# Kernel optimization log

Hardware: AMD Instinct MI355X
Metric: run time of the kernel (lower is better)

Reference implementation:

```python
import jax, jax.numpy as jnp
import numpy as np

N, E, CIN, COUT, KS, DIM = 10000, 160000, 64, 128, 5, 3
EPS = 1e-5


def spline_conv(x, src, dst, pseudo, W, Wr, bias, K):
    """SplineConv (degree=1, open spline, aggr='mean', root_weight, bias).
    x: [N, Cin]; pseudo: [E, DIM] in [0,1]; W: [K**DIM, Cin, Cout].
    For each edge, the degree-1 open B-spline basis has 2**DIM nonzero
    kernel entries. We scatter basis-weighted source features into a
    [N, K**DIM, Cin] accumulator, then contract with W in one GEMM.
    """
    n, cin = x.shape
    ktot = K ** DIM
    v = pseudo * (K - 1)                      # [E, DIM]
    bot = jnp.floor(v)
    frac = v - bot                            # fractional position in cell
    boti = bot.astype(jnp.int32)
    x_src = x[src]                            # gather [E, Cin]
    acc = jnp.zeros((n * ktot, cin), x.dtype)
    for combo in range(2 ** DIM):             # 8 fixed spline corners
        bits = [(combo >> d) & 1 for d in range(DIM)]
        w = jnp.ones((pseudo.shape[0],), x.dtype)
        idx = jnp.zeros((pseudo.shape[0],), jnp.int32)
        for d in range(DIM):
            w = w * (frac[:, d] if bits[d] else 1.0 - frac[:, d])
            idx = idx * K + jnp.clip(boti[:, d] + bits[d], 0, K - 1)
        acc = acc.at[dst * ktot + idx].add(w[:, None] * x_src)
    msg = jnp.einsum('nki,kio->no', acc.reshape(n, ktot, cin), W)
    deg = jnp.zeros((n,), x.dtype).at[dst].add(1.0)  # mean aggregation
    return msg / jnp.maximum(deg, 1.0)[:, None] + x @ Wr + bias


def batch_norm(x, g, b):
    # BatchNorm1d, training-mode batch statistics over the node dim
    mu = x.mean(0)
    var = x.var(0)
    return (x - mu) * jax.lax.rsqrt(var + EPS) * g + b


def setup_inputs() -> dict:
    key = jax.random.key(0)
    ks = jax.random.split(key, 16)
    ktot = KS ** DIM
    s1 = 1.0 / np.sqrt(CIN)
    s2 = 1.0 / np.sqrt(COUT)
    return {
        'x': jax.random.normal(ks[0], (N, CIN), jnp.float32),
        'edge_index': jax.random.randint(ks[1], (2, E), 0, N, jnp.int32),
        'edge_attr': jax.random.uniform(ks[2], (E, DIM), jnp.float32),
        'W1': jax.random.normal(ks[3], (ktot, CIN, COUT), jnp.float32) * s1,
        'Wr1': jax.random.normal(ks[4], (CIN, COUT), jnp.float32) * s1,
        'b1': jnp.zeros((COUT,), jnp.float32),
        'g1': jnp.ones((COUT,), jnp.float32),
        'be1': jnp.zeros((COUT,), jnp.float32),
        'W2': jax.random.normal(ks[5], (ktot, COUT, COUT), jnp.float32) * s2,
        'Wr2': jax.random.normal(ks[6], (COUT, COUT), jnp.float32) * s2,
        'b2': jnp.zeros((COUT,), jnp.float32),
        'g2': jnp.ones((COUT,), jnp.float32),
        'be2': jnp.zeros((COUT,), jnp.float32),
        'Wsc': jax.random.normal(ks[7], (1, CIN, COUT), jnp.float32) * s1,
        'Wrsc': jax.random.normal(ks[8], (CIN, COUT), jnp.float32) * s1,
        'bsc': jnp.zeros((COUT,), jnp.float32),
        'gsc': jnp.ones((COUT,), jnp.float32),
        'besc': jnp.zeros((COUT,), jnp.float32),
    }


def reference(x, edge_index, edge_attr, W1, Wr1, b1, g1, be1,
              W2, Wr2, b2, g2, be2, Wsc, Wrsc, bsc, gsc, besc):
    src, dst = edge_index[0], edge_index[1]
    # left branch: conv1 -> bn1 -> elu -> conv2 -> bn2
    h = spline_conv(x, src, dst, edge_attr, W1, Wr1, b1, KS)
    h = jax.nn.elu(batch_norm(h, g1, be1))
    h = batch_norm(spline_conv(h, src, dst, edge_attr, W2, Wr2, b2, KS), g2, be2)
    # shortcut: kernel_size=1 SplineConv -> bn
    s = batch_norm(spline_conv(x, src, dst, edge_attr, Wsc, Wrsc, bsc, 1), gsc, besc)
    return jax.nn.elu(h + s)
```

## Files before the change

kernel.cpp:

```cpp
#include <hip/hip_runtime.h>

#define N_NODES 10000
#define N_EDGES 160000
#define CIN 64
#define COUT 128
#define KTOT 125
#define NBINS (N_NODES * KTOT)
#define NPAIRS (N_EDGES * 8)
#define EPS 1e-5f
#define SPL 18
#define CH 3520
#define NSCB 40

#define CDIV(a,b) (((a)+(b)-1)/(b))

typedef __attribute__((ext_vector_type(8))) short short8;
typedef __attribute__((ext_vector_type(4))) float floatx4;

static __device__ __forceinline__ unsigned short f2b(float f) {
  union { float f; unsigned u; } v; v.f = f;
  unsigned r = v.u + 0x7FFFu + ((v.u >> 16) & 1u);
  return (unsigned short)(r >> 16);
}
static __device__ __forceinline__ float b2f(unsigned short u) {
  union { unsigned u; float f; } v; v.u = ((unsigned)u) << 16;
  return v.f;
}

typedef __attribute__((address_space(1))) const unsigned int guint;
typedef __attribute__((address_space(3))) unsigned int luint;
static __device__ __forceinline__ void ld_g2l16(const void* g, void* l) {
  __builtin_amdgcn_global_load_lds((guint*)g, (luint*)l, 16, 0, 0);
}

__global__ void ecount(const int* __restrict__ dst, int* __restrict__ ecnt, int E) {
  int e = blockIdx.x * 256 + threadIdx.x;
  if (e < E) atomicAdd(&ecnt[dst[e]], 1);
}

__global__ __launch_bounds__(256) void scan_blocks(const int* __restrict__ cnt,
                                                   int* __restrict__ rowptr,
                                                   int* __restrict__ cur,
                                                   int* __restrict__ bsum, int n) {
  int tid = threadIdx.x, lane = tid & 63, w = tid >> 6;
  int i = blockIdx.x * 256 + tid;
  int v = (i < n) ? cnt[i] : 0;
  int s = v;
#pragma unroll
  for (int d = 1; d < 64; d <<= 1) {
    int t = __shfl_up(s, d, 64);
    if (lane >= d) s += t;
  }
  __shared__ int ws[4];
  if (lane == 63) ws[w] = s;
  __syncthreads();
  int add = 0;
#pragma unroll
  for (int j = 0; j < 3; j++) if (w > j) add += ws[j];
  s += add;
  if (i < n) {
    rowptr[i + 1] = s;
    cur[i] = s - v;
  }
  if (tid == 255) bsum[blockIdx.x] = s;
}

__global__ __launch_bounds__(256) void scan_finish(int* __restrict__ rowptr,
                                                   int* __restrict__ cur,
                                                   const int* __restrict__ bsum, int n,
                                                   int* __restrict__ rowptr2,
                                                   float* __restrict__ stats) {
  int b = blockIdx.x, tid = threadIdx.x;
  __shared__ int offs;
  if (tid < 64) {
    int vb = (tid < b) ? bsum[tid] : 0;
#pragma unroll
    for (int d = 32; d >= 1; d >>= 1) vb += __shfl_xor(vb, d, 64);
    if (tid == 0) offs = vb;
  }
  if (b == 0) {
    for (int j = tid; j < 6 * 128; j += 256) stats[j] = 0.f;
    if (tid == 0) { rowptr[0] = 0; rowptr2[NBINS] = NPAIRS; }
  }
  __syncthreads();
  int off = offs;
  int i = b * 256 + tid;
  if (i < n) {
    rowptr[i + 1] += off;
    cur[i] += off;
  }
}

__global__ void efill(const int* __restrict__ dst, int* __restrict__ ecur,
                      int* __restrict__ eorder, int E) {
  int e = blockIdx.x * 256 + threadIdx.x;
  if (e >= E) return;
  int pos = atomicAdd(&ecur[dst[e]], 1);
  eorder[pos] = e;
}

__global__ __launch_bounds__(256) void build_pairs(
    const int* __restrict__ eorder, const int* __restrict__ erowptr,
    const int* __restrict__ src, const float* __restrict__ attr,
    int* __restrict__ rowptr2, int2* __restrict__ pairs) {
  __shared__ int hist_s[4][126];
  __shared__ int cur_s[4][126];
  int w = threadIdx.x >> 6, lane = threadIdx.x & 63;
  int node = blockIdx.x * 4 + w;
  if (node >= N_NODES) return;
  int* hist = hist_s[w];
  int* cur = cur_s[w];
  hist[lane] = 0;
  if (lane < 61) hist[64 + lane] = 0;
  __builtin_amdgcn_s_waitcnt(0);
  int e0 = erowptr[node], e1 = erowptr[node + 1];
  int deg = e1 - e0;
  float invdeg = 1.0f / fmaxf((float)deg, 1.0f);
  int sub_e = lane >> 3, corner = lane & 7;
  int bit0 = corner & 1, bit1 = (corner >> 1) & 1, bit2 = (corner >> 2) & 1;
  for (int base = 0; base < deg; base += 8) {
    int ei = base + sub_e;
    if (ei < deg) {
      int e = eorder[e0 + ei];
      float v0 = attr[e * 3 + 0] * 4.f;
      float v1 = attr[e * 3 + 1] * 4.f;
      float v2 = attr[e * 3 + 2] * 4.f;
      int i0 = (int)floorf(v0), i1 = (int)floorf(v1), i2 = (int)floorf(v2);
      int k0 = min(max(i0 + bit0, 0), 4);
      int k1 = min(max(i1 + bit1, 0), 4);
      int k2 = min(max(i2 + bit2, 0), 4);
      atomicAdd(&hist[k0 * 25 + k1 * 5 + k2], 1);
    }
  }
  __builtin_amdgcn_s_waitcnt(0);
  int v0 = hist[lane];
  int v1 = (lane < 61) ? hist[64 + lane] : 0;
  int s0 = v0;
#pragma unroll
  for (int d = 1; d < 64; d <<= 1) {
    int t = __shfl_up(s0, d, 64);
    if (lane >= d) s0 += t;
  }
  int excl0 = s0 - v0;
  int tot0 = __shfl(s0, 63, 64);
  int s1 = v1;
#pragma unroll
  for (int d = 1; d < 64; d <<= 1) {
    int t = __shfl_up(s1, d, 64);
    if (lane >= d) s1 += t;
  }
  int excl1 = s1 - v1 + tot0;
  int basep = e0 * 8;
  long rbase = (long)node * KTOT;
  rowptr2[rbase + lane] = basep + excl0;
  cur[lane] = basep + excl0;
  if (lane < 61) {
    rowptr2[rbase + 64 + lane] = basep + excl1;
    cur[64 + lane] = basep + excl1;
  }
  __builtin_amdgcn_s_waitcnt(0);
  for (int base = 0; base < deg; base += 8) {
    int ei = base + sub_e;
    if (ei < deg) {
      int e = eorder[e0 + ei];
      float v0f = attr[e * 3 + 0] * 4.f;
      float v1f = attr[e * 3 + 1] * 4.f;
      float v2f = attr[e * 3 + 2] * 4.f;
      float b0f = floorf(v0f), b1f = floorf(v1f), b2f_ = floorf(v2f);
      float f0 = v0f - b0f, f1 = v1f - b1f, f2 = v2f - b2f_;
      int i0 = (int)b0f, i1 = (int)b1f, i2 = (int)b2f_;
      float wv = (bit0 ? f0 : 1.f - f0) * (bit1 ? f1 : 1.f - f1) * (bit2 ? f2 : 1.f - f2);
      int k0 = min(max(i0 + bit0, 0), 4);
      int k1 = min(max(i1 + bit1, 0), 4);
      int k2 = min(max(i2 + bit2, 0), 4);
      int pos = atomicAdd(&cur[k0 * 25 + k1 * 5 + k2], 1);
      int2 rec; rec.x = src[e]; rec.y = __float_as_int(wv * invdeg);
      pairs[pos] = rec;
    }
  }
}

__global__ void convert_all(const float* __restrict__ x, const float* __restrict__ W1,
                            const float* __restrict__ W2, const float* __restrict__ Wr1,
                            const float* __restrict__ Wrsc, const float* __restrict__ Wr2,
                            const float* __restrict__ Wsc,
                            unsigned short* __restrict__ xb, unsigned short* __restrict__ W1aug,
                            unsigned short* __restrict__ W2t, unsigned short* __restrict__ rootBt,
                            unsigned short* __restrict__ Wr2t) {
  long i = (long)blockIdx.x * 256 + threadIdx.x;
  const long n0 = 640000, n1 = n0 + 1024000, n2 = n1 + 2048000,
             n3 = n2 + 8192, n4 = n3 + 8192, n5 = n4 + 16384, n6 = n5 + 1024000;
  if (i < n0) {
    xb[i] = f2b(x[i]);
  } else if (i < n1) {
    long j = i - n0; int k = (int)(j >> 7), c = (int)(j & 127);
    W1aug[(long)c * 8000 + k] = f2b(W1[j]);
  } else if (i < n2) {
    long j = i - n1; int k = (int)(j >> 7), c = (int)(j & 127);
    W2t[(long)c * 16000 + k] = f2b(W2[j]);
  } else if (i < n3) {
    long j = i - n2; int k = (int)(j >> 7), c = (int)(j & 127);
    rootBt[c * 64 + k] = f2b(Wr1[j]);
  } else if (i < n4) {
    long j = i - n3; int k = (int)(j >> 7), c = (int)(j & 127);
    rootBt[(128 + c) * 64 + k] = f2b(Wrsc[j]);
  } else if (i < n5) {
    long j = i - n4; int k = (int)(j >> 7), c = (int)(j & 127);
    Wr2t[c * 128 + k] = f2b(Wr2[j]);
  } else if (i < n6) {
    long j = i - n5;
    int c = (int)(j / 8000), kk = (int)(j % 8000);
    W1aug[(long)(128 + c) * 8000 + kk] = f2b(Wsc[(kk & 63) * 128 + c]);
  }
}

template<int C>
__global__ __launch_bounds__(256) void scatter_bins(
    const unsigned short* __restrict__ Xb, const int* __restrict__ rowptr2,
    const int2* __restrict__ pairs,
    unsigned short* __restrict__ accb, int bin0, int nbins_chunk) {
  int wb0 = (blockIdx.x * 4 + (threadIdx.x >> 6)) * 8;
  if (wb0 >= nbins_chunk) return;
  int lane = threadIdx.x & 63;
  int bin = bin0 + wb0;
  int bounds = 0;
  if (lane < 9) bounds = rowptr2[bin + lane];
  int b[9];
#pragma unroll
  for (int j = 0; j < 9; j++) b[j] = __shfl(bounds, j, 64);

  int sub = lane >> 5;
  int half = lane & 31;

  int pA[4], pB[4];
#pragma unroll
  for (int j = 0; j < 4; j++) {
    pA[j] = sub ? b[2 * j + 1] : b[2 * j];
    pB[j] = sub ? b[2 * j + 2] : b[2 * j + 1];
  }

  int2 r0[4], r1[4];
#pragma unroll
  for (int j = 0; j < 4; j++) {
    r0[j] = pairs[(pA[j] < pB[j]) ? pA[j] : 0];
    r1[j] = pairs[(pA[j] + 1 < pB[j]) ? (pA[j] + 1) : 0];
  }

  unsigned u0s[4], u1s[4];
  unsigned long long u0l[4], u1l[4];
#pragma unroll
  for (int j = 0; j < 4; j++) {
    if (C == 64) {
      u0s[j] = *(const unsigned*)(Xb + (long)r0[j].x * 64 + half * 2);
      u1s[j] = *(const unsigned*)(Xb + (long)r1[j].x * 64 + half * 2);
    } else {
      u0l[j] = *(const unsigned long long*)(Xb + (long)r0[j].x * 128 + half * 4);
      u1l[j] = *(const unsigned long long*)(Xb + (long)r1[j].x * 128 + half * 4);
    }
  }

#pragma unroll
  for (int j = 0; j < 4; j++) {
    int cnt = pB[j] - pA[j];
    float w0 = (cnt > 0) ? __int_as_float(r0[j].y) : 0.f;
    float w1 = (cnt > 1) ? __int_as_float(r1[j].y) : 0.f;
    float a0, a1, a2, a3;
    if (C == 64) {
      a0 = w0 * b2f((unsigned short)(u0s[j] & 0xffffu))
         + w1 * b2f((unsigned short)(u1s[j] & 0xffffu));
      a1 = w0 * b2f((unsigned short)(u0s[j] >> 16))
         + w1 * b2f((unsigned short)(u1s[j] >> 16));
      a2 = a3 = 0.f;
    } else {
      a0 = w0 * b2f((unsigned short)(u0l[j] & 0xffffu))
         + w1 * b2f((unsigned short)(u1l[j] & 0xffffu));
      a1 = w0 * b2f((unsigned short)((u0l[j] >> 16) & 0xffffu))
         + w1 * b2f((unsigned short)((u1l[j] >> 16) & 0xffffu));
      a2 = w0 * b2f((unsigned short)((u0l[j] >> 32) & 0xffffu))
         + w1 * b2f((unsigned short)((u1l[j] >> 32) & 0xffffu));
      a3 = w0 * b2f((unsigned short)(u0l[j] >> 48))
         + w1 * b2f((unsigned short)(u1l[j] >> 48));
    }
    for (int p = pA[j] + 2; p < pB[j]; p++) {
      int2 r = pairs[p];
      float w2 = __int_as_float(r.y);
      if (C == 64) {
        unsigned u = *(const unsigned*)(Xb + (long)r.x * 64 + half * 2);
        a0 += w2 * b2f((unsigned short)(u & 0xffffu));
        a1 += w2 * b2f((unsigned short)(u >> 16));
      } else {
        unsigned long long u = *(const unsigned long long*)(Xb + (long)r.x * 128 + half * 4);
        a0 += w2 * b2f((unsigned short)(u & 0xffffu));
        a1 += w2 * b2f((unsigned short)((u >> 16) & 0xffffu));
        a2 += w2 * b2f((unsigned short)((u >> 32) & 0xffffu));
        a3 += w2 * b2f((unsigned short)(u >> 48));
      }
    }
    int wb = wb0 + 2 * j + sub;
    if (wb < nbins_chunk) {
      if (C == 64) {
        unsigned pk = (unsigned)f2b(a0) | ((unsigned)f2b(a1) << 16);
        *(unsigned*)(accb + (long)wb * 64 + half * 2) = pk;
      } else {
        unsigned long long pk = (unsigned long long)((unsigned)f2b(a0) | ((unsigned)f2b(a1) << 16))
                              | ((unsigned long long)((unsigned)f2b(a2) | ((unsigned)f2b(a3) << 16)) << 32);
        *(unsigned long long*)(accb + (long)wb * 128 + half * 4) = pk;
      }
    }
  }
}

template<int NCOLS, int EC>
__global__ __launch_bounds__(256, 2) void gemm_tile(
    const unsigned short* __restrict__ A, const unsigned short* __restrict__ Aext,
    const unsigned short* __restrict__ Bt, const unsigned short* __restrict__ Bext,
    float* __restrict__ Cp, int M, int KSP) {
  __shared__ unsigned short As[4][128 * 32];
  __shared__ unsigned short Bs[4][128 * 32];
  int wid = threadIdx.x >> 6, lane = threadIdx.x & 63;
  int row0 = blockIdx.x * 128;
  int Ktot = KSP + EC;
  int nslice = gridDim.y;
  int kslice = CDIV(Ktot / 32, nslice) * 32;
  int kbeg = blockIdx.y * kslice;
  int kend = kbeg + kslice; if (kend > Ktot) kend = Ktot;
  if (kbeg >= Ktot) return;
  int nsteps = (kend - kbeg) >> 5;
  float* C = Cp + (long)blockIdx.y * M * NCOLS;

  int subsw = (lane & 3) ^ ((lane >> 3) & 3);
  int rload = lane >> 2;
  int q = lane >> 4, m16 = lane & 15;
  int sw8 = (q ^ ((m16 >> 1) & 3)) * 8;

  floatx4 acc[2][8];
#pragma unroll
  for (int t = 0; t < 2; t++)
#pragma unroll
    for (int c = 0; c < 8; c++) acc[t][c] = (floatx4){0.f, 0.f, 0.f, 0.f};

  auto stage = [&](int slot, int k0) {
    bool sp = (k0 < KSP);
    int ke = sp ? k0 : (k0 - KSP);
#pragma unroll
    for (int j = 0; j < 2; j++) {
      int tr = (wid * 2 + j) * 16 + rload;
      int gr = row0 + tr; if (gr >= M) gr = M - 1;
      const unsigned short* ap = sp ? (A + (long)gr * KSP + ke + subsw * 8)
                                    : (Aext + (long)gr * EC + ke + subsw * 8);
      const unsigned short* bp = sp ? (Bt + (long)tr * KSP + ke + subsw * 8)
                                    : (Bext + (long)tr * EC + ke + subsw * 8);
      ld_g2l16(ap, &As[slot][(wid * 2 + j) * 512]);
      ld_g2l16(bp, &Bs[slot][(wid * 2 + j) * 512]);
    }
  };

  stage(0, kbeg);
  if (nsteps > 1) stage(1, kbeg + 32);
  if (nsteps > 2) stage(2, kbeg + 64);
  int cons = 0, stg = 3;
  for (int t = 0; t < nsteps; ++t) {
    int nfut = nsteps - 1 - t;
    if (nfut >= 2) {
      asm volatile("s_waitcnt vmcnt(8)" ::: "memory");
    } else if (nfut == 1) {
      asm volatile("s_waitcnt vmcnt(4)" ::: "memory");
    } else {
      asm volatile("s_waitcnt vmcnt(0)" ::: "memory");
    }
    __builtin_amdgcn_s_barrier();
    __builtin_amdgcn_sched_barrier(0);
    if (t + 3 < nsteps) stage(stg, kbeg + (t + 3) * 32);
    const unsigned short* Ac = &As[cons][0];
    const unsigned short* Bc = &Bs[cons][0];
    short8 a0 = *(const short8*)(Ac + (wid * 32 + m16) * 32 + sw8);
    short8 a1 = *(const short8*)(Ac + (wid * 32 + 16 + m16) * 32 + sw8);
#pragma unroll
    for (int c = 0; c < 8; c++) {
      short8 b = *(const short8*)(Bc + (c * 16 + m16) * 32 + sw8);
      acc[0][c] = __builtin_amdgcn_mfma_f32_16x16x32_bf16(a0, b, acc[0][c], 0, 0, 0);
      acc[1][c] = __builtin_amdgcn_mfma_f32_16x16x32_bf16(a1, b, acc[1][c], 0, 0, 0);
    }
    __builtin_amdgcn_sched_barrier(0);
    cons = (cons + 1) & 3;
    stg = (stg + 1) & 3;
  }

#pragma unroll
  for (int t = 0; t < 2; t++) {
#pragma unroll
    for (int c = 0; c < 8; c++) {
#pragma unroll
      for (int r = 0; r < 4; r++) {
        int orow = row0 + wid * 32 + t * 16 + q * 4 + r;
        if (orow < M) C[(long)orow * NCOLS + c * 16 + m16] = acc[t][c][r];
      }
    }
  }
}

template<int EC>
__global__ __launch_bounds__(256, 2) void gemm_tile_w256(
    const unsigned short* __restrict__ A, const unsigned short* __restrict__ Aext,
    const unsigned short* __restrict__ Bt, const unsigned short* __restrict__ Bext,
    float* __restrict__ Cp, int M, int KSP) {
  __shared__ unsigned short As[3][128 * 32];
  __shared__ unsigned short Bs[3][256 * 32];
  int wid = threadIdx.x >> 6, lane = threadIdx.x & 63;
  int row0 = blockIdx.x * 128;
  int Ktot = KSP + EC;
  int nslice = gridDim.y;
  int kslice = CDIV(Ktot / 32, nslice) * 32;
  int kbeg = blockIdx.y * kslice;
  int kend = kbeg + kslice; if (kend > Ktot) kend = Ktot;
  if (kbeg >= Ktot) return;
  int nsteps = (kend - kbeg) >> 5;
  float* C = Cp + (long)blockIdx.y * M * 256;

  int subsw = (lane & 3) ^ ((lane >> 3) & 3);
  int rload = lane >> 2;
  int q = lane >> 4, m16 = lane & 15;
  int sw8 = (q ^ ((m16 >> 1) & 3)) * 8;

  floatx4 acc[2][16];
#pragma unroll
  for (int t = 0; t < 2; t++)
#pragma unroll
    for (int c = 0; c < 16; c++) acc[t][c] = (floatx4){0.f, 0.f, 0.f, 0.f};

  auto stage = [&](int slot, int k0) {
    bool sp = (k0 < KSP);
    int ke = sp ? k0 : (k0 - KSP);
#pragma unroll
    for (int j = 0; j < 2; j++) {
      int tr = (wid * 2 + j) * 16 + rload;
      int gr = row0 + tr; if (gr >= M) gr = M - 1;
      const unsigned short* ap = sp ? (A + (long)gr * KSP + ke + subsw * 8)
                                    : (Aext + (long)gr * EC + ke + subsw * 8);
      ld_g2l16(ap, &As[slot][(wid * 2 + j) * 512]);
    }
#pragma unroll
    for (int j = 0; j < 4; j++) {
      int tr = (wid * 4 + j) * 16 + rload;
      const unsigned short* bp = sp ? (Bt + (long)tr * KSP + ke + subsw * 8)
                                    : (Bext + (long)tr * EC + ke + subsw * 8);
      ld_g2l16(bp, &Bs[slot][(wid * 4 + j) * 512]);
    }
  };

  stage(0, kbeg);
  if (nsteps > 1) stage(1, kbeg + 32);
  int cons = 0, stg = 2;
  for (int t = 0; t < nsteps; ++t) {
    if (t + 1 < nsteps) {
      asm volatile("s_waitcnt vmcnt(6)" ::: "memory");
    } else {
      asm volatile("s_waitcnt vmcnt(0)" ::: "memory");
    }
    __builtin_amdgcn_s_barrier();
    __builtin_amdgcn_sched_barrier(0);
    if (t + 2 < nsteps) stage(stg, kbeg + (t + 2) * 32);
    const unsigned short* Ac = &As[cons][0];
    const unsigned short* Bc = &Bs[cons][0];
    short8 a0 = *(const short8*)(Ac + (wid * 32 + m16) * 32 + sw8);
    short8 a1 = *(const short8*)(Ac + (wid * 32 + 16 + m16) * 32 + sw8);
#pragma unroll
    for (int c = 0; c < 16; c++) {
      short8 b = *(const short8*)(Bc + (c * 16 + m16) * 32 + sw8);
      acc[0][c] = __builtin_amdgcn_mfma_f32_16x16x32_bf16(a0, b, acc[0][c], 0, 0, 0);
      acc[1][c] = __builtin_amdgcn_mfma_f32_16x16x32_bf16(a1, b, acc[1][c], 0, 0, 0);
    }
    __builtin_amdgcn_sched_barrier(0);
    if (++cons == 3) cons = 0;
    if (++stg == 3) stg = 0;
  }

#pragma unroll
  for (int t = 0; t < 2; t++) {
#pragma unroll
    for (int c = 0; c < 16; c++) {
#pragma unroll
      for (int r = 0; r < 4; r++) {
        int orow = row0 + wid * 32 + t * 16 + q * 4 + r;
        if (orow < M) C[(long)orow * 256 + c * 16 + m16] = acc[t][c][r];
      }
    }
  }
}

__global__ void reduce_finalize1(const float* __restrict__ P, const float* __restrict__ bias,
                                 float* __restrict__ h1, float* __restrict__ msgaug,
                                 float* __restrict__ stats, int cm, int c0) {
  int c = threadIdx.x;
  float bv = (c < 128) ? bias[c] : 0.f;
  float s = 0.f, s2 = 0.f;
  long tot = (long)cm * 256;
  for (long i = (long)blockIdx.x * 256 + threadIdx.x; i < tot; i += (long)gridDim.x * 256) {
    int r = (int)(i >> 8);
    float v = 0.f;
#pragma unroll
    for (int sl = 0; sl < SPL; sl++) v += P[((long)sl * cm + r) * 256 + c];
    if (c < 128) {
      v += bv;
      h1[(long)(c0 + r) * 128 + c] = v;
      s += v; s2 += v * v;
    } else {
      msgaug[(long)(c0 + r) * 256 + c] = v;
    }
  }
  if (c < 128) {
    atomicAdd(&stats[c], s);
    atomicAdd(&stats[128 + c], s2);
  }
}

__global__ void reduce_finalize2(const float* __restrict__ P, const float* __restrict__ b2,
                                 const float* __restrict__ msgaug, const float* __restrict__ bsc,
                                 float* __restrict__ h2r, float* __restrict__ sraw,
                                 float* __restrict__ stats2, float* __restrict__ statssc,
                                 int cm, int c0) {
  int c = threadIdx.x & 127;
  float bv2 = b2[c], bvsc = bsc[c];
  float sa = 0.f, sb = 0.f, ta = 0.f, tb = 0.f;
  long tot = (long)cm * 128;
  for (long i = (long)blockIdx.x * 256 + threadIdx.x; i < tot; i += (long)gridDim.x * 256) {
    int r = (int)(i >> 7);
    float v2 = 0.f;
#pragma unroll
    for (int sl = 0; sl < SPL; sl++) v2 += P[((long)sl * cm + r) * 128 + c];
    v2 += bv2;
    h2r[(long)(c0 + r) * 128 + c] = v2;
    sa += v2; sb += v2 * v2;
    float vs = msgaug[(long)(c0 + r) * 256 + 128 + c] + bvsc;
    sraw[(long)(c0 + r) * 128 + c] = vs;
    ta += vs; tb += vs * vs;
  }
  __shared__ float l0[256], l1[256], l2[256], l3[256];
  l0[threadIdx.x] = sa; l1[threadIdx.x] = sb; l2[threadIdx.x] = ta; l3[threadIdx.x] = tb;
  __syncthreads();
  if (threadIdx.x < 128) {
    atomicAdd(&stats2[c], l0[threadIdx.x] + l0[threadIdx.x + 128]);
    atomicAdd(&stats2[128 + c], l1[threadIdx.x] + l1[threadIdx.x + 128]);
    atomicAdd(&statssc[c], l2[threadIdx.x] + l2[threadIdx.x + 128]);
    atomicAdd(&statssc[128 + c], l3[threadIdx.x] + l3[threadIdx.x + 128]);
  }
}

__global__ void bn_elu_kernel(float* __restrict__ h, unsigned short* __restrict__ hb,
                              const float* __restrict__ stats, const float* __restrict__ g,
                              const float* __restrict__ be, int n) {
  long i = (long)blockIdx.x * 256 + threadIdx.x;
  if (i >= (long)n * COUT) return;
  int c = (int)(i & 127);
  float inv_n = 1.0f / n;
  float mu = stats[c] * inv_n;
  float var = stats[128 + c] * inv_n - mu * mu;
  float v = (h[i] - mu) * rsqrtf(var + EPS) * g[c] + be[c];
  v = v > 0.f ? v : expm1f(v);
  h[i] = v;
  hb[i] = f2b(v);
}

__global__ void final_out_kernel(const float* __restrict__ h2, const float* __restrict__ sraw,
                                 const float* __restrict__ st2, const float* __restrict__ stsc,
                                 const float* __restrict__ g2, const float* __restrict__ be2,
                                 const float* __restrict__ gsc, const float* __restrict__ besc,
                                 float* __restrict__ out, int n) {
  long i = (long)blockIdx.x * 256 + threadIdx.x;
  if (i >= (long)n * COUT) return;
  int c = (int)(i & 127);
  float inv_n = 1.0f / n;
  float mu2 = st2[c] * inv_n;
  float var2 = st2[128 + c] * inv_n - mu2 * mu2;
  float a = (h2[i] - mu2) * rsqrtf(var2 + EPS) * g2[c] + be2[c];
  float musc = stsc[c] * inv_n;
  float varsc = stsc[128 + c] * inv_n - musc * musc;
  float b = (sraw[i] - musc) * rsqrtf(varsc + EPS) * gsc[c] + besc[c];
  float v = a + b;
  out[i] = v > 0.f ? v : expm1f(v);
}

extern "C" void kernel_launch(void* const* d_in, const int* in_sizes, int n_in,
                              void* d_out, int out_size, void* d_ws, size_t ws_size,
                              hipStream_t stream) {
  const float* x    = (const float*)d_in[0];
  const int*   eidx = (const int*)d_in[1];
  const float* attr = (const float*)d_in[2];
  const float* W1   = (const float*)d_in[3];
  const float* Wr1  = (const float*)d_in[4];
  const float* b1   = (const float*)d_in[5];
  const float* g1   = (const float*)d_in[6];
  const float* be1  = (const float*)d_in[7];
  const float* W2   = (const float*)d_in[8];
  const float* Wr2  = (const float*)d_in[9];
  const float* b2   = (const float*)d_in[10];
  const float* g2   = (const float*)d_in[11];
  const float* be2  = (const float*)d_in[12];
  const float* Wsc  = (const float*)d_in[13];
  const float* Wrsc = (const float*)d_in[14];
  const float* bsc  = (const float*)d_in[15];
  const float* gsc  = (const float*)d_in[16];
  const float* besc = (const float*)d_in[17];
  float* out = (float*)d_out;

  const int* src = eidx;
  const int* dst = eidx + N_EDGES;

  char* base = (char*)d_ws;
  size_t off = 0;
  auto alloc = [&](size_t bytes) -> char* {
    char* p = base + off;
    off += (bytes + 255) & ~(size_t)255;
    return p;
  };
  int* ecnt   = (int*)alloc((size_t)N_NODES * 4);
  int* erowptr= (int*)alloc((size_t)(N_NODES + 1) * 4);
  int* ecur   = (int*)alloc((size_t)N_NODES * 4);
  int* eorder = (int*)alloc((size_t)N_EDGES * 4);
  int* bsum   = (int*)alloc((size_t)NSCB * 4);
  int* rowptr2= (int*)alloc((size_t)(NBINS + 1) * 4);
  int2* pairs = (int2*)alloc((size_t)NPAIRS * 8);
  unsigned short* xb    = (unsigned short*)alloc((size_t)N_NODES * CIN * 2);
  unsigned short* hb    = (unsigned short*)alloc((size_t)N_NODES * COUT * 2);
  unsigned short* W1aug = (unsigned short*)alloc((size_t)256 * KTOT * CIN * 2);
  unsigned short* W2t   = (unsigned short*)alloc((size_t)COUT * KTOT * COUT * 2);
  unsigned short* rootBt= (unsigned short*)alloc((size_t)256 * CIN * 2);
  unsigned short* Wr2t  = (unsigned short*)alloc((size_t)COUT * COUT * 2);
  float* msgaug= (float*)alloc((size_t)N_NODES * 256 * 4);
  float* h1    = (float*)alloc((size_t)N_NODES * COUT * 4);
  float* h2r   = (float*)alloc((size_t)N_NODES * COUT * 4);
  float* sraw  = (float*)alloc((size_t)N_NODES * COUT * 4);
  float* stats = (float*)alloc(6 * 128 * 4);
  char* tail = base + off;
  unsigned short* accb = (unsigned short*)tail;
  const size_t ACCB1 = (size_t)CH * KTOT * CIN * 2;
  const size_t ACCB2 = (size_t)CH * KTOT * COUT * 2;
  float* P1 = (float*)(tail + ACCB1);
  float* P2 = (float*)(tail + ACCB2);
  (void)ws_size;

  hipMemsetAsync(ecnt, 0, (size_t)N_NODES * 4, stream);

  ecount<<<CDIV(N_EDGES, 256), 256, 0, stream>>>(dst, ecnt, N_EDGES);
  scan_blocks<<<NSCB, 256, 0, stream>>>(ecnt, erowptr, ecur, bsum, N_NODES);
  scan_finish<<<NSCB, 256, 0, stream>>>(erowptr, ecur, bsum, N_NODES, rowptr2, stats);
  efill<<<CDIV(N_EDGES, 256), 256, 0, stream>>>(dst, ecur, eorder, N_EDGES);

  build_pairs<<<CDIV(N_NODES, 4), 256, 0, stream>>>(eorder, erowptr, src, attr,
                                                    rowptr2, pairs);

  const long CONV_TOT = 640000L + 1024000L + 2048000L + 8192 + 8192 + 16384 + 1024000L;
  convert_all<<<CDIV(CONV_TOT, 256), 256, 0, stream>>>(x, W1, W2, Wr1, Wrsc, Wr2, Wsc,
                                                       xb, W1aug, W2t, rootBt, Wr2t);

  for (int c0 = 0; c0 < N_NODES; c0 += CH) {
    int cm = (N_NODES - c0 < CH) ? (N_NODES - c0) : CH;
    int nbc = cm * KTOT;
    scatter_bins<64><<<CDIV(nbc, 32), 256, 0, stream>>>(xb, rowptr2, pairs, accb,
                                                        c0 * KTOT, nbc);
    dim3 g(CDIV(cm, 128), SPL);
    gemm_tile_w256<64><<<g, 256, 0, stream>>>(
        accb, xb + (size_t)c0 * CIN, W1aug, rootBt, P1, cm, KTOT * CIN);
    reduce_finalize1<<<96, 256, 0, stream>>>(P1, b1, h1, msgaug, stats, cm, c0);
  }
  bn_elu_kernel<<<CDIV(N_NODES * COUT, 256), 256, 0, stream>>>(h1, hb, stats, g1, be1, N_NODES);

  for (int c0 = 0; c0 < N_NODES; c0 += CH) {
    int cm = (N_NODES - c0 < CH) ? (N_NODES - c0) : CH;
    int nbc = cm * KTOT;
    scatter_bins<128><<<CDIV(nbc, 32), 256, 0, stream>>>(hb, rowptr2, pairs, accb,
                                                         c0 * KTOT, nbc);
    dim3 g(CDIV(cm, 128), SPL);
    gemm_tile<COUT, 128><<<g, 256, 0, stream>>>(
        accb, hb + (size_t)c0 * COUT, W2t, Wr2t, P2, cm, KTOT * COUT);
    reduce_finalize2<<<96, 256, 0, stream>>>(P2, b2, msgaug, bsc, h2r, sraw,
                                             stats + 256, stats + 512, cm, c0);
  }

  final_out_kernel<<<CDIV(N_NODES * COUT, 256), 256, 0, stream>>>(
      h2r, sraw, stats + 256, stats + 512, g2, be2, gsc, besc, out, N_NODES);
}
```

Before: 649.8 us.

## Fuse conv2 scatter-to-bins with the GEMM, building each bin tile in LDS

Replaces the chunked conv2 pipeline (scatter_bins writing a bf16 [N*125, 128] accumulator to global memory, followed by a split-K GEMM) with one kernel. Each block covers 128 nodes and 14 spline bins. For each bin it gathers the basis-weighted neighbour features straight into LDS and multiplies them against the matching W2 slice with MFMA, and the root weight is handled as an extra bin. This removes the large global round trip of the bin accumulator and the per-chunk launches. In exchange there is no multi-stage pipelining: each bin step does a synchronous gather, then barriers, then compute, and the K split drops from 18 to 9 slices.

After: 707.3 us. 1.09x slower.

```diff
diff --git a/kernel.cpp b/kernel.cpp
--- a/kernel.cpp
+++ b/kernel.cpp
@@ -9,6 +9,7 @@
 #define NPAIRS (N_EDGES * 8)
 #define EPS 1e-5f
 #define SPL 18
+#define SPL2 9
 #define CH 3520
 #define NSCB 40
 
@@ -310,28 +311,17 @@
   }
 }
 
-template<int NCOLS, int EC>
-__global__ __launch_bounds__(256, 2) void gemm_tile(
-    const unsigned short* __restrict__ A, const unsigned short* __restrict__ Aext,
-    const unsigned short* __restrict__ Bt, const unsigned short* __restrict__ Bext,
-    float* __restrict__ Cp, int M, int KSP) {
-  __shared__ unsigned short As[4][128 * 32];
-  __shared__ unsigned short Bs[4][128 * 32];
+__global__ __launch_bounds__(256, 2) void fused_conv2(
+    const unsigned short* __restrict__ Hb, const int* __restrict__ rowptr2,
+    const int2* __restrict__ pairs, const unsigned short* __restrict__ W2t,
+    const unsigned short* __restrict__ Wr2t, float* __restrict__ Cp, int M) {
+  __shared__ unsigned short Asl[128 * 128];
+  __shared__ unsigned short Bsl[128 * 128];
   int wid = threadIdx.x >> 6, lane = threadIdx.x & 63;
-  int row0 = blockIdx.x * 128;
-  int Ktot = KSP + EC;
-  int nslice = gridDim.y;
-  int kslice = CDIV(Ktot / 32, nslice) * 32;
-  int kbeg = blockIdx.y * kslice;
-  int kend = kbeg + kslice; if (kend > Ktot) kend = Ktot;
-  if (kbeg >= Ktot) return;
-  int nsteps = (kend - kbeg) >> 5;
-  float* C = Cp + (long)blockIdx.y * M * NCOLS;
-
-  int subsw = (lane & 3) ^ ((lane >> 3) & 3);
-  int rload = lane >> 2;
+  int r0 = blockIdx.x * 128;
+  int kb0 = blockIdx.y * 14;
   int q = lane >> 4, m16 = lane & 15;
-  int sw8 = (q ^ ((m16 >> 1) & 3)) * 8;
+  int sub = lane >> 5, half = lane & 31;
 
   floatx4 acc[2][8];
 #pragma unroll
@@ -339,61 +329,119 @@
 #pragma unroll
     for (int c = 0; c < 8; c++) acc[t][c] = (floatx4){0.f, 0.f, 0.f, 0.f};
 
-  auto stage = [&](int slot, int k0) {
-    bool sp = (k0 < KSP);
-    int ke = sp ? k0 : (k0 - KSP);
-#pragma unroll
-    for (int j = 0; j < 2; j++) {
-      int tr = (wid * 2 + j) * 16 + rload;
-      int gr = row0 + tr; if (gr >= M) gr = M - 1;
-      const unsigned short* ap = sp ? (A + (long)gr * KSP + ke + subsw * 8)
-                                    : (Aext + (long)gr * EC + ke + subsw * 8);
-      const unsigned short* bp = sp ? (Bt + (long)tr * KSP + ke + subsw * 8)
-                                    : (Bext + (long)tr * EC + ke + subsw * 8);
-      ld_g2l16(ap, &As[slot][(wid * 2 + j) * 512]);
-      ld_g2l16(bp, &Bs[slot][(wid * 2 + j) * 512]);
-    }
-  };
-
-  stage(0, kbeg);
-  if (nsteps > 1) stage(1, kbeg + 32);
-  if (nsteps > 2) stage(2, kbeg + 64);
-  int cons = 0, stg = 3;
-  for (int t = 0; t < nsteps; ++t) {
-    int nfut = nsteps - 1 - t;
-    if (nfut >= 2) {
-      asm volatile("s_waitcnt vmcnt(8)" ::: "memory");
-    } else if (nfut == 1) {
-      asm volatile("s_waitcnt vmcnt(4)" ::: "memory");
+  int bnode = r0 + wid * 32 + (lane >> 1);
+  if (bnode >= M) bnode = M - 1;
+
+  for (int kk = 0; kk < 14; ++kk) {
+    int kbin = kb0 + kk;
+    {
+      char* ldst = (char*)Bsl + wid * 8192 + lane * 16;
+      if (kbin < KTOT) {
+        const unsigned short* wbp = W2t + (long)kbin * 128;
+#pragma unroll
+        for (int k = 0; k < 8; k++) {
+          int tr = wid * 32 + k * 4 + (lane >> 4);
+          int sc = (lane & 15) ^ (tr & 15);
+          ld_g2l16(wbp + (long)tr * 16000 + sc * 8, ldst + k * 1024);
+        }
+      } else {
+#pragma unroll
+        for (int k = 0; k < 8; k++) {
+          int tr = wid * 32 + k * 4 + (lane >> 4);
+          int sc = (lane & 15) ^ (tr & 15);
+          ld_g2l16(Wr2t + (long)tr * 128 + sc * 8, ldst + k * 1024);
+        }
+      }
+    }
+    if (kbin < KTOT) {
+      int v = rowptr2[(long)bnode * KTOT + kbin + (lane & 1)];
+#pragma unroll
+      for (int g = 0; g < 4; g++) {
+        int pAa[4], pBa[4];
+#pragma unroll
+        for (int jj = 0; jj < 4; jj++) {
+          int jl = g * 8 + 2 * jj + sub;
+          pAa[jj] = __shfl(v, 2 * jl, 64);
+          pBa[jj] = __shfl(v, 2 * jl + 1, 64);
+        }
+        int2 rv0[4], rv1[4];
+#pragma unroll
+        for (int jj = 0; jj < 4; jj++) {
+          rv0[jj] = pairs[(pAa[jj] < pBa[jj]) ? pAa[jj] : 0];
+          rv1[jj] = pairs[(pAa[jj] + 1 < pBa[jj]) ? (pAa[jj] + 1) : 0];
+        }
+        unsigned long long u0[4], u1[4];
+#pragma unroll
+        for (int jj = 0; jj < 4; jj++) {
+          u0[jj] = *(const unsigned long long*)(Hb + (long)rv0[jj].x * 128 + half * 4);
+          u1[jj] = *(const unsigned long long*)(Hb + (long)rv1[jj].x * 128 + half * 4);
+        }
+#pragma unroll
+        for (int jj = 0; jj < 4; jj++) {
+          int cnt = pBa[jj] - pAa[jj];
+          float w0 = (cnt > 0) ? __int_as_float(rv0[jj].y) : 0.f;
+          float w1 = (cnt > 1) ? __int_as_float(rv1[jj].y) : 0.f;
+          float a0 = w0 * b2f((unsigned short)(u0[jj] & 0xffffu))
+                   + w1 * b2f((unsigned short)(u1[jj] & 0xffffu));
+          float a1 = w0 * b2f((unsigned short)((u0[jj] >> 16) & 0xffffu))
+                   + w1 * b2f((unsigned short)((u1[jj] >> 16) & 0xffffu));
+          float a2 = w0 * b2f((unsigned short)((u0[jj] >> 32) & 0xffffu))
+                   + w1 * b2f((unsigned short)((u1[jj] >> 32) & 0xffffu));
+          float a3 = w0 * b2f((unsigned short)(u0[jj] >> 48))
+                   + w1 * b2f((unsigned short)(u1[jj] >> 48));
+          for (int p = pAa[jj] + 2; p < pBa[jj]; p++) {
+            int2 r = pairs[p];
+            float w2 = __int_as_float(r.y);
+            unsigned long long u = *(const unsigned long long*)(Hb + (long)r.x * 128 + half * 4);
+            a0 += w2 * b2f((unsigned short)(u & 0xffffu));
+            a1 += w2 * b2f((unsigned short)((u >> 16) & 0xffffu));
+            a2 += w2 * b2f((unsigned short)((u >> 32) & 0xffffu));
+            a3 += w2 * b2f((unsigned short)(u >> 48));
+          }
+          unsigned long long pk = (unsigned long long)((unsigned)f2b(a0) | ((unsigned)f2b(a1) << 16))
+                                | ((unsigned long long)((unsigned)f2b(a2) | ((unsigned)f2b(a3) << 16)) << 32);
+          int wb = wid * 32 + g * 8 + 2 * jj + sub;
+          *(unsigned long long*)((char*)Asl + wb * 256 +
+              (((half >> 1) ^ (wb & 15)) << 4) + (half & 1) * 8) = pk;
+        }
+      }
     } else {
-      asm volatile("s_waitcnt vmcnt(0)" ::: "memory");
-    }
-    __builtin_amdgcn_s_barrier();
-    __builtin_amdgcn_sched_barrier(0);
-    if (t + 3 < nsteps) stage(stg, kbeg + (t + 3) * 32);
-    const unsigned short* Ac = &As[cons][0];
-    const unsigned short* Bc = &Bs[cons][0];
-    short8 a0 = *(const short8*)(Ac + (wid * 32 + m16) * 32 + sw8);
-    short8 a1 = *(const short8*)(Ac + (wid * 32 + 16 + m16) * 32 + sw8);
+      int row = threadIdx.x >> 1;
+      int node = r0 + row;
+      int nc = (node < M) ? node : M - 1;
+      int cb = (threadIdx.x & 1) * 8;
+#pragma unroll
+      for (int i = 0; i < 8; i++) {
+        int c16 = cb + i;
+        short8 hv = *(const short8*)(Hb + (long)nc * 128 + c16 * 8);
+        *(short8*)((char*)Asl + row * 256 + ((c16 ^ (row & 15)) << 4)) = hv;
+      }
+    }
+    __syncthreads();
+#pragma unroll
+    for (int ks = 0; ks < 4; ks++) {
+      int cs = ks * 4 + q;
+      short8 a0 = *(const short8*)((char*)Asl + (wid * 32 + m16) * 256 + ((cs ^ m16) << 4));
+      short8 a1 = *(const short8*)((char*)Asl + (wid * 32 + 16 + m16) * 256 + ((cs ^ m16) << 4));
+#pragma unroll
+      for (int c = 0; c < 8; c++) {
+        short8 b = *(const short8*)((char*)Bsl + (c * 16 + m16) * 256 + ((cs ^ m16) << 4));
+        acc[0][c] = __builtin_amdgcn_mfma_f32_16x16x32_bf16(a0, b, acc[0][c], 0, 0, 0);
+        acc[1][c] = __builtin_amdgcn_mfma_f32_16x16x32_bf16(a1, b, acc[1][c], 0, 0, 0);
+      }
+    }
+    __syncthreads();
+  }
+
+  float* C = Cp + (long)blockIdx.y * M * COUT;
+#pragma unroll
+  for (int t = 0; t < 2; t++) {
 #pragma unroll
     for (int c = 0; c < 8; c++) {
-      short8 b = *(const short8*)(Bc + (c * 16 + m16) * 32 + sw8);
-      acc[0][c] = __builtin_amdgcn_mfma_f32_16x16x32_bf16(a0, b, acc[0][c], 0, 0, 0);
-      acc[1][c] = __builtin_amdgcn_mfma_f32_16x16x32_bf16(a1, b, acc[1][c], 0, 0, 0);
-    }
-    __builtin_amdgcn_sched_barrier(0);
-    cons = (cons + 1) & 3;
-    stg = (stg + 1) & 3;
-  }
-
-#pragma unroll
-  for (int t = 0; t < 2; t++) {
-#pragma unroll
-    for (int c = 0; c < 8; c++) {
 #pragma unroll
       for (int r = 0; r < 4; r++) {
-        int orow = row0 + wid * 32 + t * 16 + q * 4 + r;
-        if (orow < M) C[(long)orow * NCOLS + c * 16 + m16] = acc[t][c][r];
+        int orow = r0 + wid * 32 + t * 16 + q * 4 + r;
+        if (orow < M) C[(long)orow * COUT + c * 16 + m16] = acc[t][c][r];
       }
     }
   }
@@ -527,7 +575,7 @@
     int r = (int)(i >> 7);
     float v2 = 0.f;
 #pragma unroll
-    for (int sl = 0; sl < SPL; sl++) v2 += P[((long)sl * cm + r) * 128 + c];
+    for (int sl = 0; sl < SPL2; sl++) v2 += P[((long)sl * cm + r) * 128 + c];
     v2 += bv2;
     h2r[(long)(c0 + r) * 128 + c] = v2;
     sa += v2; sb += v2 * v2;
@@ -634,9 +682,8 @@
   char* tail = base + off;
   unsigned short* accb = (unsigned short*)tail;
   const size_t ACCB1 = (size_t)CH * KTOT * CIN * 2;
-  const size_t ACCB2 = (size_t)CH * KTOT * COUT * 2;
-  float* P1 = (float*)(tail + ACCB1);
-  float* P2 = (float*)(tail + ACCB2);
+  float* P1  = (float*)(tail + ACCB1);
+  float* P2f = (float*)tail;
   (void)ws_size;
 
   hipMemsetAsync(ecnt, 0, (size_t)N_NODES * 4, stream);
@@ -665,16 +712,11 @@
   }
   bn_elu_kernel<<<CDIV(N_NODES * COUT, 256), 256, 0, stream>>>(h1, hb, stats, g1, be1, N_NODES);
 
-  for (int c0 = 0; c0 < N_NODES; c0 += CH) {
-    int cm = (N_NODES - c0 < CH) ? (N_NODES - c0) : CH;
-    int nbc = cm * KTOT;
-    scatter_bins<128><<<CDIV(nbc, 32), 256, 0, stream>>>(hb, rowptr2, pairs, accb,
-                                                         c0 * KTOT, nbc);
-    dim3 g(CDIV(cm, 128), SPL);
-    gemm_tile<COUT, 128><<<g, 256, 0, stream>>>(
-        accb, hb + (size_t)c0 * COUT, W2t, Wr2t, P2, cm, KTOT * COUT);
-    reduce_finalize2<<<96, 256, 0, stream>>>(P2, b2, msgaug, bsc, h2r, sraw,
-                                             stats + 256, stats + 512, cm, c0);
+  {
+    dim3 gf(CDIV(N_NODES, 128), SPL2);
+    fused_conv2<<<gf, 256, 0, stream>>>(hb, rowptr2, pairs, W2t, Wr2t, P2f, N_NODES);
+    reduce_finalize2<<<192, 256, 0, stream>>>(P2f, b2, msgaug, bsc, h2r, sraw,
+                                              stats + 256, stats + 512, N_NODES, 0);
   }
 
   final_out_kernel<<<CDIV(N_NODES * COUT, 256), 256, 0, stream>>>(
```
